# Kernel optimization log

Hardware: AMD Instinct MI355X
Metric: run time of the kernel (lower is better)

## Reference

```python
import jax, jax.numpy as jnp
import numpy as np

N_FILTERS = 40
FILTER_SIZE = 401   # int(16000*25/1000), forced odd
POOL_STRIDE = 160   # int(16000*10/1000)
EPS = 1e-6
S_SMOOTH = 0.04     # fixed PCEN smoothing coefficient s
DELTA = 2.0         # fixed PCEN bias delta
R_MIN, R_MAX = 0.2, 1.0
HIDDEN = 32


def setup_inputs() -> dict:
    key = jax.random.key(0)
    ks = jax.random.split(key, 6)
    B, L = 8, 160000
    x = jax.random.normal(ks[0], (B, L), dtype=jnp.float32)
    # mel-initialized Gabor params (as in mel_filter_params)
    sr, fmin, fmax = 16000.0, 60.0, 7800.0
    min_mel = 1127.0 * np.log1p(fmin / 700.0)
    max_mel = 1127.0 * np.log1p(fmax / 700.0)
    peaks_mel = np.linspace(min_mel, max_mel, N_FILTERS + 2)
    peaks_hz = 700.0 * np.expm1(peaks_mel / 1127.0)
    center_freqs = jnp.asarray(peaks_hz[1:-1] * 2.0 * np.pi / sr, dtype=jnp.float32)
    z = np.sqrt(2.0 * np.log(2.0)) / np.pi
    bandwidths = jnp.asarray(z * sr / (peaks_hz[2:] - peaks_hz[:-2]), dtype=jnp.float32)
    pooling_widths = jnp.full((N_FILTERS,), 0.4, dtype=jnp.float32)
    # GRU (input_size=1, hidden=32) + head Linear(32,32)->ReLU->Linear(32,2)
    def gl(k, shape):
        return jax.random.normal(k, shape, dtype=jnp.float32) * 0.1
    w_ih = gl(ks[1], (3 * HIDDEN, 1))
    w_hh = gl(ks[2], (3 * HIDDEN, HIDDEN))
    b_ih = jnp.zeros((3 * HIDDEN,), jnp.float32)
    b_hh = jnp.zeros((3 * HIDDEN,), jnp.float32)
    hw1 = gl(ks[3], (32, HIDDEN)); hb1 = jnp.zeros((32,), jnp.float32)
    hw2 = gl(ks[4], (2, 32)); hb2 = jnp.zeros((2,), jnp.float32)
    return dict(x=x, center_freqs=center_freqs, bandwidths=bandwidths,
                pooling_widths=pooling_widths, w_ih=w_ih, w_hh=w_hh,
                b_ih=b_ih, b_hh=b_hh, hw1=hw1, hb1=hb1, hw2=hw2, hb2=hb2)


def _gabor_filterbank(x, center_freqs, bandwidths, pooling_widths):
    z = np.sqrt(2.0 * np.log(2.0)) / np.pi
    cf = jnp.clip(center_freqs, 0.0, np.pi)
    bw = jnp.clip(bandwidths, 4.0 * z, FILTER_SIZE * z)
    t = jnp.arange(-(FILTER_SIZE // 2), (FILTER_SIZE + 1) // 2, dtype=jnp.float32)
    denom = 1.0 / (jnp.sqrt(2.0 * np.pi) * bw)                        # [F]
    gauss = jnp.exp(-(t[None, :] ** 2) / (2.0 * bw[:, None] ** 2))    # [F,K]
    phase = cf[:, None] * t[None, :]                                  # [F,K]
    fr = denom[:, None] * gauss * jnp.cos(phase)
    fi = denom[:, None] * gauss * jnp.sin(phase)
    filt = jnp.concatenate([fr, fi], axis=0)[:, None, :]              # [2F,1,K]
    pad = FILTER_SIZE // 2
    y = jax.lax.conv_general_dilated(x[:, None, :], filt, (1,), [(pad, pad)])
    y = y ** 2
    y = y[:, :N_FILTERS] + y[:, N_FILTERS:]                           # squared modulus [B,F,L]
    pw = jnp.clip(pooling_widths, 2.0 / FILTER_SIZE, 0.5)
    tt = jnp.arange(FILTER_SIZE, dtype=jnp.float32) / (FILTER_SIZE - 1) - 0.5
    win = jnp.exp(-0.5 * (tt[None, :] / pw[:, None]) ** 2)[:, None, :]  # [F,1,K]
    y = jax.lax.conv_general_dilated(y, win, (POOL_STRIDE,), [(pad, pad)],
                                     feature_group_count=N_FILTERS)
    return y  # [B,F,T]


def _gru_cell(h, xin, w_ih, w_hh, b_ih, b_hh):
    gi = xin @ w_ih.T + b_ih   # [N,3H]
    gh = h @ w_hh.T + b_hh
    i_r, i_z, i_n = jnp.split(gi, 3, axis=-1)
    h_r, h_z, h_n = jnp.split(gh, 3, axis=-1)
    r = jax.nn.sigmoid(i_r + h_r)
    zz = jax.nn.sigmoid(i_z + h_z)
    n = jnp.tanh(i_n + r * h_n)
    return (1.0 - zz) * n + zz * h


def _adaptive_pcen(frames, w_ih, w_hh, b_ih, b_hh, hw1, hb1, hw2, hb2):
    B, F, T = frames.shape
    Xt = jnp.transpose(frames, (2, 0, 1))  # [T,B,F]

    def controller(x_prev, x_t):  # each [B,F] -> per-bin (alpha, r)
        xp = x_prev.reshape(-1, 1)
        xc = x_t.reshape(-1, 1)
        h = jnp.zeros((B * F, HIDDEN), frames.dtype)
        h = _gru_cell(h, xp, w_ih, w_hh, b_ih, b_hh)
        h = _gru_cell(h, xc, w_ih, w_hh, b_ih, b_hh)
        hid = jax.nn.relu(h @ hw1.T + hb1)
        logits = hid @ hw2.T + hb2  # [B*F,2]
        alpha = jax.nn.sigmoid(logits[:, 0]).reshape(B, F)
        r = (R_MIN + (R_MAX - R_MIN) * jax.nn.sigmoid(logits[:, 1])).reshape(B, F)
        return alpha, r

    def step(carry, X_t):
        M_prev, X_prev = carry
        alpha, r = controller(X_prev, X_t)
        M_t = (1.0 - S_SMOOTH) * M_prev + S_SMOOTH * X_t
        out = (X_t / (M_t + EPS) ** alpha + DELTA) ** r - DELTA ** r
        return (M_t, X_t), out

    init = (jnp.zeros((B, F), frames.dtype), Xt[0])
    _, outs = jax.lax.scan(step, init, Xt)
    return jnp.transpose(outs, (1, 2, 0))  # [B,F,T]


def reference(x, center_freqs, bandwidths, pooling_widths,
              w_ih, w_hh, b_ih, b_hh, hw1, hb1, hw2, hb2):
    frames = _gabor_filterbank(x, center_freqs, bandwidths, pooling_widths)
    return _adaptive_pcen(frames, w_ih, w_hh, b_ih, b_hh, hw1, hb1, hw2, hb2)
```

## Files before the change

kernel.cpp:

```cpp
#include <hip/hip_runtime.h>
#include <math.h>

#define NF 40
#define FS 401
#define AST 424
#define PSTRIDE 160
#define BB 8
#define LL 160000
#define PADL 256
#define PADR 512
#define LST 160768
#define TOUT 1000
#define NTILE 512
#define NCHUNKC 313
#define ROWCH 121
#define ROWST (ROWCH*8)
#define TCP 16
#define NCHUNKP 63
#define NCONVB 5024

typedef __attribute__((ext_vector_type(8))) _Float16 half8v;
typedef __attribute__((ext_vector_type(4))) _Float16 half4v;
typedef __attribute__((ext_vector_type(4))) float float4v;
typedef _Float16 f16;

__device__ __forceinline__ float sigm(float x) { return 1.0f / (1.0f + __expf(-x)); }
__device__ __forceinline__ float tanh_fast(float x) { return 1.0f - 2.0f / (__expf(2.0f * x) + 1.0f); }

__global__ __launch_bounds__(256) void prep_all(
    const float* __restrict__ x, const float* __restrict__ cf_,
    const float* __restrict__ bw_, f16* __restrict__ xb, f16* __restrict__ Ag)
{
    int blk = blockIdx.x;
    if (blk < NCONVB) {
        int i = blk * 256 + threadIdx.x;
        int b = i / LST, o = i % LST;
        float v = 0.0f;
        if (o >= PADL && o < PADL + LL) v = x[b * LL + (o - PADL)];
        xb[i] = (f16)v;
        return;
    }
    const float PI_F = 3.14159265358979323846f;
    int row = blk - NCONVB;
    int f = row >> 1, comp = row & 1;
    float Z = sqrtf(2.0f * logf(2.0f)) / PI_F;
    float cf = fminf(fmaxf(cf_[f], 0.0f), PI_F);
    float bw = fminf(fmaxf(bw_[f], 4.0f * Z), 401.0f * Z);
    float denom = 1.0f / (sqrtf(2.0f * PI_F) * bw);
    float inv2 = 1.0f / (2.0f * bw * bw);
    for (int k = threadIdx.x; k < AST; k += 256) {
        float v = 0.0f;
        if (k < FS) {
            float t = (float)(k - 200);
            float g = denom * expf(-(t * t) * inv2);
            float sv, cv;
            sincosf(cf * t, &sv, &cv);
            v = comp ? g * sv : g * cv;
        }
        Ag[row * AST + k] = (f16)v;
    }
}

__global__ __launch_bounds__(256, 2) void conv_mfma(
    const f16* __restrict__ xb,
    const f16* __restrict__ Ag,
    f16* __restrict__ eb)
{
    __shared__ f16 slab[8 * ROWST];
    int chunk = blockIdx.x;
    int bi = blockIdx.y;
    int p0 = chunk * NTILE;
    int pbase = PADL + p0 - 200;
    const f16* xs = xb + (size_t)bi * LST;
    int tid = threadIdx.x;

    for (int sc = tid; sc < 8 * 117; sc += 256) {
        int r = sc / 117, m = sc - r * 117;
        int s0 = pbase + 8 * m + (r & ~1);
        const uint* gp = (const uint*)(xs + s0);
        uint v0 = gp[0], v1 = gp[1], v2 = gp[2], v3 = gp[3], v4 = gp[4];
        if (r & 1) {
            v0 = __builtin_amdgcn_alignbyte(v1, v0, 2);
            v1 = __builtin_amdgcn_alignbyte(v2, v1, 2);
            v2 = __builtin_amdgcn_alignbyte(v3, v2, 2);
            v3 = __builtin_amdgcn_alignbyte(v4, v3, 2);
        }
        *(uint4*)(&slab[r * ROWST + 8 * m]) = make_uint4(v0, v1, v2, v3);
    }
    __syncthreads();

    int wv = tid >> 6, lane = tid & 63, q = lane >> 4, l15 = lane & 15;

    float4v acc[5][8];
#pragma unroll
    for (int t = 0; t < 5; ++t)
#pragma unroll
        for (int s = 0; s < 8; ++s)
            acc[t][s] = (float4v){0.f, 0.f, 0.f, 0.f};

    const f16* aP[5];
    const f16* bP[8];
#pragma unroll
    for (int t = 0; t < 5; ++t) aP[t] = Ag + (16 * t + l15) * AST + 8 * q;
#pragma unroll
    for (int s = 0; s < 8; ++s) {
        int pos = 128 * wv + 16 * s + l15;
        bP[s] = slab + (pos & 7) * ROWST + 8 * ((pos >> 3) + q);
    }

    for (int k = 0; k < 416; k += 32) {
        half8v af[5], bf[8];
#pragma unroll
        for (int t = 0; t < 5; ++t) af[t] = *(const half8v*)(aP[t] + k);
#pragma unroll
        for (int s = 0; s < 8; ++s) bf[s] = *(const half8v*)(bP[s] + k);
#pragma unroll
        for (int t = 0; t < 5; ++t)
#pragma unroll
            for (int s = 0; s < 8; ++s)
                acc[t][s] = __builtin_amdgcn_mfma_f32_16x16x32_f16(af[t], bf[s], acc[t][s], 0, 0, 0);
    }

    f16* ebb = eb + (size_t)bi * NF * LL;
#pragma unroll
    for (int t = 0; t < 5; ++t) {
        int f0 = 8 * t + 2 * q;
#pragma unroll
        for (int s = 0; s < 8; ++s) {
            float4v a = acc[t][s];
            int p = p0 + 128 * wv + 16 * s + l15;
            if (p < LL) {
                ebb[f0 * LL + p] = (f16)(a.x * a.x + a.y * a.y);
                ebb[(f0 + 1) * LL + p] = (f16)(a.z * a.z + a.w * a.w);
            }
        }
    }
}

__global__ __launch_bounds__(256) void pool_kernel(
    const f16* __restrict__ eb, const float* __restrict__ pw_, float* __restrict__ Xout)
{
    __shared__ float ys[2816];
    __shared__ float win[416];
    int chunk = blockIdx.x;
    int f = blockIdx.y;
    int bi = blockIdx.z;
    int tau0 = chunk * TCP;
    int start = tau0 * PSTRIDE - 200;
    int tid = threadIdx.x;

    float pw = fminf(fmaxf(pw_[f], 2.0f / 401.0f), 0.5f);
    float invpw = 1.0f / pw;
    for (int k = tid; k < 416; k += 256) {
        float w = 0.0f;
        if (k < FS) {
            float tt = (float)k * (1.0f / 400.0f) - 0.5f;
            float u = tt * invpw;
            w = expf(-0.5f * u * u);
        }
        win[k] = w;
    }
    const f16* erow = eb + ((size_t)bi * NF + f) * LL;
    if (start >= 0 && start + 2816 <= LL) {
        for (int j = tid; j < 352; j += 256) {
            half8v v = *(const half8v*)(erow + start + 8 * j);
#pragma unroll
            for (int i = 0; i < 8; ++i) ys[8 * j + i] = (float)v[i];
        }
    } else {
        for (int j = tid; j < 2816; j += 256) {
            int p = start + j;
            ys[j] = (p >= 0 && p < LL) ? (float)erow[p] : 0.0f;
        }
    }
    __syncthreads();

    int ft = tid >> 4, l16 = tid & 15;
    float acc = 0.0f;
    int yo = ft * PSTRIDE;
    for (int kw = l16; kw < FS; kw += 16)
        acc += ys[yo + kw] * win[kw];
#pragma unroll
    for (int off = 8; off > 0; off >>= 1)
        acc += __shfl_down(acc, off, 16);
    int tau = tau0 + ft;
    if (l16 == 0 && tau < TOUT)
        Xout[((size_t)bi * NF + f) * TOUT + tau] = acc;
}

__global__ __launch_bounds__(256) void pcen_scan_kernel(
    const float* __restrict__ X, float* __restrict__ M)
{
    int wid = (blockIdx.x * 256 + threadIdx.x) >> 6;
    int lane = threadIdx.x & 63;
    if (wid >= BB * NF) return;
    const float a1 = 0.96f;
    const float a2 = a1 * a1;
    const float a4 = a2 * a2;
    const float a8 = a4 * a4;
    const float a16 = a8 * a8;
    const float a32 = a16 * a16;
    const float ss = 0.04f;
    float al1 = powf(a1, (float)(lane + 1));
    float carry = 0.0f;
    const float* row = X + wid * TOUT;
    float* mrow = M + wid * TOUT;

    for (int c = 0; c < TOUT; c += 64) {
        int t = c + lane;
        float v = (t < TOUT) ? row[t] : 0.0f;
        float y = ss * v;
        float u;
        u = __shfl_up(y, 1, 64);  if (lane >= 1)  y = fmaf(a1, u, y);
        u = __shfl_up(y, 2, 64);  if (lane >= 2)  y = fmaf(a2, u, y);
        u = __shfl_up(y, 4, 64);  if (lane >= 4)  y = fmaf(a4, u, y);
        u = __shfl_up(y, 8, 64);  if (lane >= 8)  y = fmaf(a8, u, y);
        u = __shfl_up(y, 16, 64); if (lane >= 16) y = fmaf(a16, u, y);
        u = __shfl_up(y, 32, 64); if (lane >= 32) y = fmaf(a32, u, y);
        y = fmaf(al1, carry, y);
        carry = __shfl(y, 63, 64);
        if (t < TOUT) mrow[t] = y;
    }
}

__global__ __launch_bounds__(256) void pcen_ctrl_mfma(
    const float* __restrict__ X, const float* __restrict__ M,
    const float* __restrict__ w_ih, const float* __restrict__ w_hh,
    const float* __restrict__ b_ih, const float* __restrict__ b_hh,
    const float* __restrict__ hw1, const float* __restrict__ hb1,
    const float* __restrict__ hw2, const float* __restrict__ hb2,
    float* __restrict__ out)
{
    __shared__ f16 s_whhA[96 * 40];
    __shared__ f16 s_w1A[32 * 40];
    __shared__ __align__(16) float4 s_A1[32];
    __shared__ __align__(16) float4 s_A2[32];
    __shared__ float s_hb1[32];
    __shared__ float s_hw2[64];
    __shared__ float s_hb2[2];
    __shared__ f16 sh1[4][16 * 40];
    __shared__ f16 sh2[4][16 * 40];
    __shared__ float sxc[4][16], sxp[4][16], smv[4][16];

    int tid = threadIdx.x;
    for (int i = tid; i < 96 * 32; i += 256) {
        int m = i >> 5, k = i & 31;
        s_whhA[m * 40 + k] = (f16)w_hh[i];
    }
    for (int i = tid; i < 32 * 32; i += 256) {
        int m = i >> 5, k = i & 31;
        s_w1A[m * 40 + k] = (f16)hw1[i];
    }
    if (tid < 32) {
        int j = tid;
        s_A1[j] = make_float4(w_ih[j], b_ih[j] + b_hh[j],
                              w_ih[32 + j], b_ih[32 + j] + b_hh[32 + j]);
        s_A2[j] = make_float4(w_ih[64 + j], b_ih[64 + j], b_hh[64 + j], 0.0f);
        s_hb1[j] = hb1[j];
    }
    if (tid < 64) s_hw2[tid] = hw2[tid];
    if (tid < 2)  s_hb2[tid] = hb2[tid];
    __syncthreads();

    int wv = tid >> 6, lane = tid & 63;
    int c = lane & 15, q = lane >> 4;
    int instBase = blockIdx.x * 64 + wv * 16;

    if (lane < 16) {
        int idx = instBase + lane;
        int t = idx % TOUT;
        float xcv = X[idx];
        float xpv = (t == 0) ? xcv : X[idx - 1];
        sxc[wv][lane] = xcv;
        sxp[wv][lane] = xpv;
        smv[wv][lane] = M[idx];
    }
    float xp = sxp[wv][c];
    float xc = sxc[wv][c];
    float mv = smv[wv][c];

    float h1v[8];
#pragma unroll
    for (int jj = 0; jj < 8; ++jj) {
        int j = (jj < 4) ? (4 * q + jj) : (16 + 4 * q + (jj - 4));
        float4 a1 = s_A1[j];
        float4 a2 = s_A2[j];
        float r = sigm(fmaf(xp, a1.x, a1.y));
        float z = sigm(fmaf(xp, a1.z, a1.w));
        float n = tanh_fast(fmaf(xp, a2.x, a2.y) + r * a2.z);
        h1v[jj] = (1.0f - z) * n;
    }

    {
        half4v lo = {(f16)h1v[0], (f16)h1v[1], (f16)h1v[2], (f16)h1v[3]};
        half4v hi = {(f16)h1v[4], (f16)h1v[5], (f16)h1v[6], (f16)h1v[7]};
        *(half4v*)(&sh1[wv][c * 40 + 4 * q]) = lo;
        *(half4v*)(&sh1[wv][c * 40 + 16 + 4 * q]) = hi;
    }

    float4v acc[6];
    {
        half8v bf = *(const half8v*)(&sh1[wv][c * 40 + 8 * q]);
#pragma unroll
        for (int t = 0; t < 6; ++t) {
            half8v af = *(const half8v*)(&s_whhA[(16 * t + c) * 40 + 8 * q]);
            acc[t] = __builtin_amdgcn_mfma_f32_16x16x32_f16(af, bf, (float4v){0.f,0.f,0.f,0.f}, 0, 0, 0);
        }
    }

    float h2v[8];
#pragma unroll
    for (int jj = 0; jj < 8; ++jj) {
        int j = (jj < 4) ? (4 * q + jj) : (16 + 4 * q + (jj - 4));
        int reg = jj & 3;
        float accR = (jj < 4) ? acc[0][reg] : acc[1][reg];
        float accZ = (jj < 4) ? acc[2][reg] : acc[3][reg];
        float accN = (jj < 4) ? acc[4][reg] : acc[5][reg];
        float4 a1 = s_A1[j];
        float4 a2 = s_A2[j];
        float r = sigm(fmaf(xc, a1.x, a1.y) + accR);
        float z = sigm(fmaf(xc, a1.z, a1.w) + accZ);
        float gn = accN + a2.z;
        float n = tanh_fast(fmaf(xc, a2.x, a2.y) + r * gn);
        h2v[jj] = fmaf(z, h1v[jj] - n, n);
    }

    {
        half4v lo = {(f16)h2v[0], (f16)h2v[1], (f16)h2v[2], (f16)h2v[3]};
        half4v hi = {(f16)h2v[4], (f16)h2v[5], (f16)h2v[6], (f16)h2v[7]};
        *(half4v*)(&sh2[wv][c * 40 + 4 * q]) = lo;
        *(half4v*)(&sh2[wv][c * 40 + 16 + 4 * q]) = hi;
    }

    float4v hacc[2];
    {
        half8v bf = *(const half8v*)(&sh2[wv][c * 40 + 8 * q]);
#pragma unroll
        for (int t = 0; t < 2; ++t) {
            half8v af = *(const half8v*)(&s_w1A[(16 * t + c) * 40 + 8 * q]);
            hacc[t] = __builtin_amdgcn_mfma_f32_16x16x32_f16(af, bf, (float4v){0.f,0.f,0.f,0.f}, 0, 0, 0);
        }
    }

    float p0 = 0.f, p1 = 0.f;
#pragma unroll
    for (int jj = 0; jj < 8; ++jj) {
        int i = (jj < 4) ? (4 * q + jj) : (16 + 4 * q + (jj - 4));
        int reg = jj & 3;
        float hv = (jj < 4) ? hacc[0][reg] : hacc[1][reg];
        hv = fmaxf(hv + s_hb1[i], 0.0f);
        p0 = fmaf(hv, s_hw2[i], p0);
        p1 = fmaf(hv, s_hw2[32 + i], p1);
    }
    p0 += __shfl_xor(p0, 16);
    p0 += __shfl_xor(p0, 32);
    p1 += __shfl_xor(p1, 16);
    p1 += __shfl_xor(p1, 32);

    float alpha = sigm(p0 + s_hb2[0]);
    float rr = fmaf(0.8f, sigm(p1 + s_hb2[1]), 0.2f);
    float md = __expf(alpha * __logf(mv + 1e-6f));
    float bse = xc / md + 2.0f;
    float val = __expf(rr * __logf(bse)) - __expf(rr * 0.69314718056f);
    if (lane < 16)
        out[instBase + lane] = val;
}

extern "C" void kernel_launch(void* const* d_in, const int* in_sizes, int n_in,
                              void* d_out, int out_size, void* d_ws, size_t ws_size,
                              hipStream_t stream) {
    const float* x    = (const float*)d_in[0];
    const float* cf   = (const float*)d_in[1];
    const float* bw   = (const float*)d_in[2];
    const float* pw   = (const float*)d_in[3];
    const float* w_ih = (const float*)d_in[4];
    const float* w_hh = (const float*)d_in[5];
    const float* b_ih = (const float*)d_in[6];
    const float* b_hh = (const float*)d_in[7];
    const float* hw1  = (const float*)d_in[8];
    const float* hb1  = (const float*)d_in[9];
    const float* hw2  = (const float*)d_in[10];
    const float* hb2  = (const float*)d_in[11];
    float* out = (float*)d_out;

    const size_t xb_b = (size_t)BB * LST * 2;
    const size_t ag_b = (size_t)80 * AST * 2;
    const size_t xm_b = (size_t)2 * BB * NF * TOUT * 4;
    size_t fixed = xb_b + ag_b + xm_b;
    size_t e_per_batch = (size_t)NF * LL * 2;
    int nb;
    if (ws_size >= fixed + 8 * e_per_batch)      nb = 8;
    else if (ws_size >= fixed + 2 * e_per_batch) nb = 2;
    else                                         nb = 1;
    int nslice = BB / nb;

    f16* xb   = (f16*)d_ws;
    f16* Ag   = xb + (size_t)BB * LST;
    f16* ebuf = Ag + (size_t)80 * AST;
    float* Xf = (float*)(ebuf + (size_t)nb * NF * LL);
    float* Mf = Xf + (size_t)BB * NF * TOUT;

    prep_all<<<dim3(NCONVB + 80), dim3(256), 0, stream>>>(x, cf, bw, xb, Ag);

    for (int sl = 0; sl < nslice; ++sl) {
        conv_mfma<<<dim3(NCHUNKC, nb), dim3(256), 0, stream>>>(
            xb + (size_t)sl * nb * LST, Ag, ebuf);
        pool_kernel<<<dim3(NCHUNKP, NF, nb), dim3(256), 0, stream>>>(
            ebuf, pw, Xf + (size_t)sl * nb * NF * TOUT);
    }

    pcen_scan_kernel<<<dim3((BB * NF * 64) / 256), dim3(256), 0, stream>>>(Xf, Mf);
    pcen_ctrl_mfma<<<dim3((BB * NF * TOUT) / 64), dim3(256), 0, stream>>>(
        Xf, Mf, w_ih, w_hh, b_ih, b_hh, hw1, hb1, hw2, hb2, out);
}
```

Before: 310.8 us.

## Stage conv energy output through LDS for coalesced stores and reuse B fragments

The MFMA convolution kernel now writes its squared-magnitude results into a shared-memory tile, then stores them to global memory as 16-byte coalesced vectors instead of scattered 2-byte stores. The k-loop is fully unrolled and exploits the Toeplitz structure: B fragments shift by two per k-step, so only two new fragments are loaded from LDS per iteration instead of eight. The slab load and input padding grow to cover the extra positions. This adds shared memory usage and extra barriers, and the full unroll raises register pressure.

```diff
diff --git a/kernel.cpp b/kernel.cpp
--- a/kernel.cpp
+++ b/kernel.cpp
@@ -8,16 +8,16 @@
 #define BB 8
 #define LL 160000
 #define PADL 256
-#define PADR 512
-#define LST 160768
+#define LST 161024
 #define TOUT 1000
 #define NTILE 512
 #define NCHUNKC 313
 #define ROWCH 121
 #define ROWST (ROWCH*8)
+#define EROW 520
 #define TCP 16
 #define NCHUNKP 63
-#define NCONVB 5024
+#define NCONVB 5032
 
 typedef __attribute__((ext_vector_type(8))) _Float16 half8v;
 typedef __attribute__((ext_vector_type(4))) _Float16 half4v;
@@ -66,7 +66,10 @@
     const f16* __restrict__ Ag,
     f16* __restrict__ eb)
 {
-    __shared__ f16 slab[8 * ROWST];
+    __shared__ __align__(16) unsigned char smem[40 * EROW * 2];
+    f16* slab = (f16*)smem;
+    f16* eL   = (f16*)smem;
+
     int chunk = blockIdx.x;
     int bi = blockIdx.y;
     int p0 = chunk * NTILE;
@@ -74,8 +77,8 @@
     const f16* xs = xb + (size_t)bi * LST;
     int tid = threadIdx.x;
 
-    for (int sc = tid; sc < 8 * 117; sc += 256) {
-        int r = sc / 117, m = sc - r * 117;
+    for (int sc = tid; sc < 8 * 120; sc += 256) {
+        int r = sc / 120, m = sc - r * 120;
         int s0 = pbase + 8 * m + (r & ~1);
         const uint* gp = (const uint*)(xs + s0);
         uint v0 = gp[0], v1 = gp[1], v2 = gp[2], v3 = gp[3], v4 = gp[4];
@@ -99,40 +102,66 @@
             acc[t][s] = (float4v){0.f, 0.f, 0.f, 0.f};
 
     const f16* aP[5];
-    const f16* bP[8];
+    const f16* bPtr[10];
 #pragma unroll
     for (int t = 0; t < 5; ++t) aP[t] = Ag + (16 * t + l15) * AST + 8 * q;
 #pragma unroll
-    for (int s = 0; s < 8; ++s) {
+    for (int s = 0; s < 10; ++s) {
         int pos = 128 * wv + 16 * s + l15;
-        bP[s] = slab + (pos & 7) * ROWST + 8 * ((pos >> 3) + q);
-    }
-
-    for (int k = 0; k < 416; k += 32) {
-        half8v af[5], bf[8];
+        bPtr[s] = slab + (pos & 7) * ROWST + 8 * ((pos >> 3) + q);
+    }
+
+    half8v bf[8];
+#pragma unroll
+    for (int s = 0; s < 8; ++s) bf[s] = *(const half8v*)(bPtr[s]);
+
+#pragma unroll
+    for (int kk = 0; kk < 13; ++kk) {
+        int k = 32 * kk;
+        half8v af[5];
 #pragma unroll
         for (int t = 0; t < 5; ++t) af[t] = *(const half8v*)(aP[t] + k);
-#pragma unroll
-        for (int s = 0; s < 8; ++s) bf[s] = *(const half8v*)(bP[s] + k);
+        half8v nb0, nb1;
+        if (kk < 12) {
+            nb0 = *(const half8v*)(bPtr[8] + k);
+            nb1 = *(const half8v*)(bPtr[9] + k);
+        }
 #pragma unroll
         for (int t = 0; t < 5; ++t)
 #pragma unroll
             for (int s = 0; s < 8; ++s)
                 acc[t][s] = __builtin_amdgcn_mfma_f32_16x16x32_f16(af[t], bf[s], acc[t][s], 0, 0, 0);
-    }
-
-    f16* ebb = eb + (size_t)bi * NF * LL;
+        if (kk < 12) {
+#pragma unroll
+            for (int s = 0; s < 6; ++s) bf[s] = bf[s + 2];
+            bf[6] = nb0; bf[7] = nb1;
+        }
+    }
+
+    __syncthreads();
+
 #pragma unroll
     for (int t = 0; t < 5; ++t) {
         int f0 = 8 * t + 2 * q;
 #pragma unroll
         for (int s = 0; s < 8; ++s) {
             float4v a = acc[t][s];
-            int p = p0 + 128 * wv + 16 * s + l15;
-            if (p < LL) {
-                ebb[f0 * LL + p] = (f16)(a.x * a.x + a.y * a.y);
-                ebb[(f0 + 1) * LL + p] = (f16)(a.z * a.z + a.w * a.w);
-            }
+            int pl = 128 * wv + 16 * s + l15;
+            eL[f0 * EROW + pl] = (f16)(a.x * a.x + a.y * a.y);
+            eL[(f0 + 1) * EROW + pl] = (f16)(a.z * a.z + a.w * a.w);
+        }
+    }
+    __syncthreads();
+
+    f16* ebb = eb + (size_t)bi * NF * LL;
+#pragma unroll
+    for (int it = 0; it < 10; ++it) {
+        int idx = it * 256 + tid;
+        int row = idx >> 6;
+        int off = (idx & 63) * 8;
+        if (p0 + off < LL) {
+            uint4 v = *(const uint4*)(&eL[row * EROW + off]);
+            *(uint4*)(&ebb[row * LL + p0 + off]) = v;
         }
     }
 }
```

New measurement: 260.7 us. 16.1% less time.
